# Optimization experiments

Measured on AMD Instinct MI355X. Metric: run time of the kernel, lower is better.

## Reference

```python
import jax, jax.numpy as jnp
import numpy as np

# Production-scale graph dims (see shape_source)
N = 50000      # nodes
E = 800000     # edges (avg degree 16)
C_IN = 128     # input feature dim
H = 96         # hidden (per species: prey X and predator Y)
C_OUT = 40     # num_classes
L = 5          # LVConv layers
DT = 0.05      # integration step


def setup_inputs() -> dict:
    key = jax.random.key(0)
    ks = jax.random.split(key, 14)
    x = jax.random.normal(ks[0], (N, C_IN), jnp.float32)
    edge_index = jax.random.randint(ks[1], (2, E), 0, N, dtype=jnp.int32)
    # lift linears
    Wx = jax.random.normal(ks[2], (C_IN, H), jnp.float32) / np.sqrt(C_IN)
    bx = jnp.zeros((H,), jnp.float32)
    Wy = jax.random.normal(ks[3], (C_IN, H), jnp.float32) / np.sqrt(C_IN)
    by = jnp.zeros((H,), jnp.float32)
    # per-layer Lotka-Volterra coefficients (per-channel), small positive scale
    alpha = 0.1 * jax.random.uniform(ks[4], (L, H), jnp.float32)
    beta  = 0.1 * jax.random.uniform(ks[5], (L, H), jnp.float32)
    gamma = 0.1 * jax.random.uniform(ks[6], (L, H), jnp.float32)
    delta = 0.1 * jax.random.uniform(ks[7], (L, H), jnp.float32)
    # readout on concat([X, Y])
    Wr = jax.random.normal(ks[8], (2 * H, C_OUT), jnp.float32) / np.sqrt(2 * H)
    br = jnp.zeros((C_OUT,), jnp.float32)
    return {"x": x, "edge_index": edge_index, "Wx": Wx, "bx": bx,
            "Wy": Wy, "by": by, "alpha": alpha, "beta": beta,
            "gamma": gamma, "delta": delta, "Wr": Wr, "br": br}


def reference(x, edge_index, Wx, bx, Wy, by, alpha, beta, gamma, delta, Wr, br):
    src, dst = edge_index[0], edge_index[1]
    # in-degree for mean aggregation over incoming edges
    deg = jax.ops.segment_sum(jnp.ones((E,), x.dtype), dst, num_segments=N)
    deg_inv = (1.0 / jnp.maximum(deg, 1.0))[:, None]  # [N,1]

    def mean_agg(v):  # [N,H] -> [N,H] neighbor mean (src -> dst)
        return jax.ops.segment_sum(v[src], dst, num_segments=N) * deg_inv

    # lift to prey (X) and predator (Y) populations
    X = jnp.tanh(x @ Wx + bx)
    Y = jnp.tanh(x @ Wy + by)
    # dropout is identity in eval mode (training=False)
    for l in range(L):
        aggX = mean_agg(X)
        aggY = mean_agg(Y)
        # explicit-Euler Lotka-Volterra dynamics on the graph
        Xn = X + DT * X * (alpha[l] - beta[l] * aggY)
        Yn = Y + DT * Y * (-gamma[l] + delta[l] * aggX)
        X, Y = Xn, Yn
    h = jnp.concatenate([X, Y], axis=-1)  # [N, 2H]
    return h @ Wr + br
```

## Files before the change

### kernel.cpp

```cpp
#include <hip/hip_runtime.h>
#include <hip/hip_bf16.h>
#include <hip/hip_fp16.h>


#define HDIM 96
#define CIN 128
#define COUT 40
#define NLAYER 5
#define DTC 0.05f

#define BK_SHIFT 7
#define BK_SIZE 128
#define EPB 2048
#define BCAP 3072
#define BSTRIDE 3584

typedef float  vfloat2 __attribute__((ext_vector_type(2)));
typedef float  vfloat4 __attribute__((ext_vector_type(4)));
typedef short  vshort8 __attribute__((ext_vector_type(8)));

__device__ __forceinline__ unsigned bf16_rne(float f) {
    unsigned u = __float_as_uint(f);
    return (u + 0x7fffu + ((u >> 16) & 1u)) >> 16;
}

__device__ __forceinline__ unsigned pack_bf16_pair(float xf, float yf) {
    return bf16_rne(xf) | (bf16_rne(yf) << 16);
}

__device__ __forceinline__ unsigned pack_f16_pair(float a, float b) {
    unsigned ha = (unsigned)__half_as_ushort(__float2half_rn(a));
    unsigned hb = (unsigned)__half_as_ushort(__float2half_rn(b));
    return ha | (hb << 16);
}

__device__ __forceinline__ float f16_lo(unsigned u) {
    return __half2float(__ushort_as_half((unsigned short)(u & 0xffffu)));
}
__device__ __forceinline__ float f16_hi(unsigned u) {
    return __half2float(__ushort_as_half((unsigned short)(u >> 16)));
}

__device__ __forceinline__ unsigned pack_fp8_quad(float x0, float y0, float x1, float y1) {
    int lo = __builtin_amdgcn_cvt_pk_fp8_f32(x0, y0, 0, false);
    int full = __builtin_amdgcn_cvt_pk_fp8_f32(x1, y1, lo, true);
    return (unsigned)full;
}

__device__ __forceinline__ float fast_tanh(float x) {
    float e = __expf(2.0f * x);
    return 1.0f - 2.0f * __builtin_amdgcn_rcpf(e + 1.0f);
}


__global__ __launch_bounds__(256) void wprep_kernel(
    const float* __restrict__ Wx, const float* __restrict__ bx,
    const float* __restrict__ Wy, const float* __restrict__ by,
    unsigned short* __restrict__ WcT, float* __restrict__ bc,
    int* __restrict__ gcur, int NB,
    unsigned* __restrict__ Fz0, unsigned* __restrict__ Fz1) {
    int t = blockIdx.x * blockDim.x + threadIdx.x;
    if (t < NB) gcur[t] = 0;
    if (t < 192 * 128) {
        int cc = t >> 7;
        int k = t & 127;
        int h = cc >> 1;
        float w = (cc & 1) ? Wy[k * HDIM + h] : Wx[k * HDIM + h];
        WcT[cc * 128 + k] = (unsigned short)bf16_rne(w);
    }
    if (t < 192) {
        int h = t >> 1;
        bc[t] = (t & 1) ? by[h] : bx[h];
    }
    if (blockIdx.x == 0 && threadIdx.x < 48) {
        Fz0[threadIdx.x] = 0u;
        Fz1[threadIdx.x] = 0u;
    }
}


__global__ __launch_bounds__(256) void bscatter_kernel(
    const int* __restrict__ src, const int* __restrict__ dst,
    int* __restrict__ gcur, unsigned* __restrict__ packed, int E, int NB) {
    __shared__ int h[512];
    __shared__ int cur[512];
    for (int i = threadIdx.x; i < NB; i += 256) h[i] = 0;
    __syncthreads();
    int base = blockIdx.x * EPB;
    int end = min(E, base + EPB);
    for (int e = base + threadIdx.x; e < end; e += 256)
        atomicAdd(&h[dst[e] >> BK_SHIFT], 1);
    __syncthreads();
    for (int i = threadIdx.x; i < NB; i += 256)
        cur[i] = h[i] ? atomicAdd(&gcur[i], h[i]) : 0;
    __syncthreads();
    for (int e = base + threadIdx.x; e < end; e += 256) {
        int d = dst[e];
        int b = d >> BK_SHIFT;
        int pos = atomicAdd(&cur[b], 1);
        if (pos < BCAP)
            packed[(size_t)b * BCAP + pos] =
                (unsigned)src[e] | ((unsigned)(d & (BK_SIZE - 1)) << 17);
    }
}


__global__ __launch_bounds__(256) void bcsr_kernel(
    const unsigned* __restrict__ packed, const int* __restrict__ gcur,
    uint2* __restrict__ rowinfo, int* __restrict__ csr, int N, int NB) {
    __shared__ int ldeg[BK_SIZE];
    __shared__ int sscan[BK_SIZE];
    __shared__ int lcur[BK_SIZE];
    int b = blockIdx.x;
    int t = threadIdx.x;
    int cnt = min(gcur[b], BCAP);
    const unsigned* pk = packed + (size_t)b * BCAP;
    int wbase = b * BSTRIDE;
    if (t < BK_SIZE) ldeg[t] = 0;
    __syncthreads();
    for (int e = t; e < cnt; e += 256)
        atomicAdd(&ldeg[(pk[e] >> 17) & (BK_SIZE - 1)], 1);
    __syncthreads();
    int deg = 0, pad = 0;
    if (t < BK_SIZE) {
        deg = ldeg[t];
        pad = (deg + 3) & ~3;
        sscan[t] = pad;
    }
    __syncthreads();
    for (int off = 1; off < BK_SIZE; off <<= 1) {
        int tv = (t < BK_SIZE && t >= off) ? sscan[t - off] : 0;
        __syncthreads();
        if (t < BK_SIZE) sscan[t] += tv;
        __syncthreads();
    }
    int gpos = 0;
    if (t < BK_SIZE) {
        gpos = wbase + sscan[t] - pad;
        lcur[t] = gpos;
        int node = b * BK_SIZE + t;
        if (node < N) {
            rowinfo[node] = make_uint2(
                (unsigned)gpos | ((unsigned)(pad >> 2) << 21),
                __float_as_uint(1.0f / fmaxf((float)deg, 1.0f)));
        }
    }
    __syncthreads();
    for (int e = t; e < cnt; e += 256) {
        unsigned p = pk[e];
        int l = (p >> 17) & (BK_SIZE - 1);
        int pos = atomicAdd(&lcur[l], 1);
        csr[pos] = (int)(p & 0x1FFFFu);
    }
    __syncthreads();
    if (t < BK_SIZE) {
        for (int p = lcur[t]; p < gpos + pad; p++) csr[p] = N;
    }
}


#define LW_STRIDE 136
#define TILE_STRIDE 200

__global__ __launch_bounds__(256) void lift_mfma_kernel(
    const float* __restrict__ x, const unsigned short* __restrict__ WcT,
    const float* __restrict__ bc, unsigned* __restrict__ S,
    unsigned* __restrict__ F, int N) {
    __shared__ __align__(16) char smem[192 * LW_STRIDE * 2];
    __shared__ float sBc[192];
    unsigned short* sW = (unsigned short*)smem;
    unsigned short* tile = (unsigned short*)smem;
    int t = threadIdx.x;

    {
        const unsigned* g = (const unsigned*)WcT;
        unsigned* s = (unsigned*)sW;
        for (int i = t; i < 192 * 64; i += 256) {
            int cc = i >> 6;
            int kp = i & 63;
            s[cc * (LW_STRIDE / 2) + kp] = g[i];
        }
    }
    if (t < 192) sBc[t] = bc[t];
    __syncthreads();

    int wv = t >> 6;
    int lane = t & 63;
    int quad = lane >> 4;
    int m = lane & 15;
    int mbase = blockIdx.x * 64 + wv * 16;

    int anode = mbase + m;
    if (anode >= N) anode = N - 1;
    const float* xrow = x + (size_t)anode * CIN;

    vfloat4 acc[12];
#pragma unroll
    for (int i = 0; i < 12; i++) acc[i] = (vfloat4){0.f, 0.f, 0.f, 0.f};

#pragma unroll
    for (int kt = 0; kt < 4; kt++) {
        int k0 = kt * 32 + quad * 8;
        float4 xa = *(const float4*)(xrow + k0);
        float4 xb = *(const float4*)(xrow + k0 + 4);
        uint4 ua;
        ua.x = pack_bf16_pair(xa.x, xa.y);
        ua.y = pack_bf16_pair(xa.z, xa.w);
        ua.z = pack_bf16_pair(xb.x, xb.y);
        ua.w = pack_bf16_pair(xb.z, xb.w);
        vshort8 a = *(vshort8*)&ua;
#pragma unroll
        for (int nt = 0; nt < 12; nt++) {
            vshort8 b = *(const vshort8*)&sW[(nt * 16 + m) * LW_STRIDE + k0];
            acc[nt] = __builtin_amdgcn_mfma_f32_16x16x32_bf16(a, b, acc[nt], 0, 0, 0);
        }
    }

    __syncthreads();
#pragma unroll
    for (int nt = 0; nt < 12; nt++) {
        int ccb = nt * 16 + m;
        float bco = sBc[ccb];
#pragma unroll
        for (int r = 0; r < 4; r++) {
            int nl = wv * 16 + quad * 4 + r;
            float v = fast_tanh(acc[nt][r] + bco);
            tile[nl * TILE_STRIDE + ccb] = __half_as_ushort(__float2half_rn(v));
        }
    }
    __syncthreads();

    int nbase = blockIdx.x * 64;
#pragma unroll
    for (int i = 0; i < 6; i++) {
        int idx = i * 256 + t;
        int nl = idx / 24;
        int pos = idx - nl * 24;
        int node = nbase + nl;
        uint4 u = *(const uint4*)&tile[nl * TILE_STRIDE + pos * 8];
        if (node < N) {
            *(uint4*)(S + (size_t)node * 96 + pos * 4) = u;
            float f0 = f16_lo(u.x), f1 = f16_hi(u.x);
            float f2 = f16_lo(u.y), f3 = f16_hi(u.y);
            float f4 = f16_lo(u.z), f5 = f16_hi(u.z);
            float f6 = f16_lo(u.w), f7 = f16_hi(u.w);
            uint2 fq = make_uint2(pack_fp8_quad(f0, f1, f2, f3),
                                  pack_fp8_quad(f4, f5, f6, f7));
            *(uint2*)(F + (size_t)node * 48 + pos * 2) = fq;
        }
    }
}


__global__ __launch_bounds__(256) void layer_kernel(
    const unsigned* __restrict__ F, const unsigned* __restrict__ S,
    unsigned* __restrict__ Sn, unsigned* __restrict__ Fn,
    const uint2* __restrict__ rowinfo, const int* __restrict__ csr,
    const float* __restrict__ alpha, const float* __restrict__ beta,
    const float* __restrict__ gamma, const float* __restrict__ delta,
    int N) {
    int wave = threadIdx.x >> 6;
    int lane = threadIdx.x & 63;
    int li = lane & 15;
    int gbase = lane & 48;

    int node = (blockIdx.x * 4 + wave) * 4 + (lane >> 4);
    bool nvalid = node < N;
    int nclamp = nvalid ? node : N - 1;
    uint2 ri = rowinfo[nclamp];
    int beg = (int)(ri.x & 0x1FFFFFu);
    int cnt = nvalid ? (int)((ri.x >> 21) << 2) : 0;
    float dinv = __uint_as_float(ri.y);

    const uint2* srow = (const uint2*)(S + (size_t)nclamp * 96);
    uint2 su0 = srow[3 * li + 0];
    uint2 su1 = srow[3 * li + 1];
    uint2 su2 = srow[3 * li + 2];

    vfloat2 ac2[6];
#pragma unroll
    for (int i = 0; i < 6; i++) ac2[i] = (vfloat2){0.f, 0.f};

#define UNP(u, k)                                                           \
    do {                                                                    \
        vfloat2 p0 = __builtin_amdgcn_cvt_pk_f32_fp8((int)(u), false);      \
        vfloat2 p1 = __builtin_amdgcn_cvt_pk_f32_fp8((int)(u), true);       \
        ac2[2*(k)+0] += p0; ac2[2*(k)+1] += p1;                             \
    } while (0)
#define UNP3(u)  do { UNP((u).x, 0); UNP((u).y, 1); UNP((u).z, 2); } while (0)

    for (int base = 0; base < cnt; base += 64) {
        int rem = min(cnt - base, 64);
        int4 my = {0, 0, 0, 0};
        if (li * 4 < rem) my = *(const int4*)(csr + beg + base + 4 * li);
        int j = 0;
        for (; j + 8 <= rem; j += 8) {
            int l0 = gbase + (j >> 2);
            int s0 = __shfl(my.x, l0);
            int s1 = __shfl(my.y, l0);
            int s2 = __shfl(my.z, l0);
            int s3 = __shfl(my.w, l0);
            int s4 = __shfl(my.x, l0 + 1);
            int s5 = __shfl(my.y, l0 + 1);
            int s6 = __shfl(my.z, l0 + 1);
            int s7 = __shfl(my.w, l0 + 1);
            uint3 u0 = ((const uint3*)(F + (size_t)s0 * 48))[li];
            uint3 u1 = ((const uint3*)(F + (size_t)s1 * 48))[li];
            uint3 u2 = ((const uint3*)(F + (size_t)s2 * 48))[li];
            uint3 u3 = ((const uint3*)(F + (size_t)s3 * 48))[li];
            uint3 u4 = ((const uint3*)(F + (size_t)s4 * 48))[li];
            uint3 u5 = ((const uint3*)(F + (size_t)s5 * 48))[li];
            uint3 u6 = ((const uint3*)(F + (size_t)s6 * 48))[li];
            uint3 u7 = ((const uint3*)(F + (size_t)s7 * 48))[li];
            UNP3(u0); UNP3(u1); UNP3(u2); UNP3(u3);
            UNP3(u4); UNP3(u5); UNP3(u6); UNP3(u7);
        }
        if (j < rem) {
            int l0 = gbase + (j >> 2);
            int s0 = __shfl(my.x, l0);
            int s1 = __shfl(my.y, l0);
            int s2 = __shfl(my.z, l0);
            int s3 = __shfl(my.w, l0);
            uint3 u0 = ((const uint3*)(F + (size_t)s0 * 48))[li];
            uint3 u1 = ((const uint3*)(F + (size_t)s1 * 48))[li];
            uint3 u2 = ((const uint3*)(F + (size_t)s2 * 48))[li];
            uint3 u3 = ((const uint3*)(F + (size_t)s3 * 48))[li];
            UNP3(u0); UNP3(u1); UNP3(u2); UNP3(u3);
        }
    }
#undef UNP3
#undef UNP

    if (!nvalid) return;

    unsigned so[6];
    unsigned fo[3];
#pragma unroll
    for (int k = 0; k < 3; k++) {
        int p = 3 * li + k;
        float2 a2 = ((const float2*)alpha)[p];
        float2 b2 = ((const float2*)beta)[p];
        float2 g2 = ((const float2*)gamma)[p];
        float2 d2 = ((const float2*)delta)[p];
        uint2 su = (k == 0) ? su0 : (k == 1) ? su1 : su2;
        float vx = f16_lo(su.x), vy = f16_hi(su.x);
        float vz = f16_lo(su.y), vw = f16_hi(su.y);
        float ox = vx + DTC * vx * (a2.x - b2.x * (ac2[2*k].y * dinv));
        float oy = vy + DTC * vy * (-g2.x + d2.x * (ac2[2*k].x * dinv));
        float oz = vz + DTC * vz * (a2.y - b2.y * (ac2[2*k+1].y * dinv));
        float ow = vw + DTC * vw * (-g2.y + d2.y * (ac2[2*k+1].x * dinv));
        so[2*k+0] = pack_f16_pair(ox, oy);
        so[2*k+1] = pack_f16_pair(oz, ow);
        fo[k] = pack_fp8_quad(ox, oy, oz, ow);
    }
    {
        uint3 t0 = {so[0], so[1], so[2]};
        uint3 t1 = {so[3], so[4], so[5]};
        ((uint3*)(Sn + (size_t)node * 96))[2*li+0] = t0;
        ((uint3*)(Sn + (size_t)node * 96))[2*li+1] = t1;
    }
    if (Fn) {
        uint3 tf = {fo[0], fo[1], fo[2]};
        ((uint3*)(Fn + (size_t)node * 48))[li] = tf;
    }
}


#define WG_STRIDE 200

__global__ __launch_bounds__(256) void readout_mfma_kernel(
    const unsigned short* __restrict__ sh, const float* __restrict__ Wr,
    const float* __restrict__ br, float* __restrict__ out, int N) {
    __shared__ unsigned short sW[48 * WG_STRIDE];
    __shared__ float sB[48];
    int t = threadIdx.x;

    for (int i = t; i < 48 * 192; i += 256) {
        int n = i / 192;
        int kk = i - n * 192;
        int h = kk >> 1;
        float w = 0.f;
        if (n < COUT) w = (kk & 1) ? Wr[(HDIM + h) * COUT + n] : Wr[h * COUT + n];
        sW[n * WG_STRIDE + kk] = __half_as_ushort(__float2half_rn(w));
    }
    if (t < 48) sB[t] = (t < COUT) ? br[t] : 0.f;
    __syncthreads();

    int wv = t >> 6;
    int lane = t & 63;
    int quad = lane >> 4;
    int m = lane & 15;
    int mbase = blockIdx.x * 64 + wv * 16;

    int anode = mbase + m;
    if (anode >= N) anode = N - 1;
    const unsigned short* arow = sh + (size_t)anode * 192;

    vfloat4 acc0 = {0.f, 0.f, 0.f, 0.f};
    vfloat4 acc1 = {0.f, 0.f, 0.f, 0.f};
    vfloat4 acc2 = {0.f, 0.f, 0.f, 0.f};

#pragma unroll
    for (int kt = 0; kt < 6; kt++) {
        int k0 = kt * 32 + quad * 8;
        vshort8 a = *(const vshort8*)(arow + k0);
        vshort8 b0 = *(const vshort8*)&sW[(0 * 16 + m) * WG_STRIDE + k0];
        vshort8 b1 = *(const vshort8*)&sW[(1 * 16 + m) * WG_STRIDE + k0];
        vshort8 b2 = *(const vshort8*)&sW[(2 * 16 + m) * WG_STRIDE + k0];
        acc0 = __builtin_amdgcn_mfma_f32_16x16x32_f16(a, b0, acc0, 0, 0, 0);
        acc1 = __builtin_amdgcn_mfma_f32_16x16x32_f16(a, b1, acc1, 0, 0, 0);
        acc2 = __builtin_amdgcn_mfma_f32_16x16x32_f16(a, b2, acc2, 0, 0, 0);
    }

    float bo0 = sB[m];
    float bo1 = sB[16 + m];
    float bo2 = (m < 8) ? sB[32 + m] : 0.f;
#pragma unroll
    for (int r = 0; r < 4; r++) {
        int node = mbase + quad * 4 + r;
        if (node < N) {
            float* orow = out + (size_t)node * COUT;
            orow[m] = acc0[r] + bo0;
            orow[16 + m] = acc1[r] + bo1;
            if (m < 8) orow[32 + m] = acc2[r] + bo2;
        }
    }
}


extern "C" void kernel_launch(void* const* d_in, const int* in_sizes, int n_in,
                              void* d_out, int out_size, void* d_ws, size_t ws_size,
                              hipStream_t stream) {
    const float* x     = (const float*)d_in[0];
    const int*   ei    = (const int*)d_in[1];
    const float* Wx    = (const float*)d_in[2];
    const float* bx    = (const float*)d_in[3];
    const float* Wy    = (const float*)d_in[4];
    const float* by    = (const float*)d_in[5];
    const float* alpha = (const float*)d_in[6];
    const float* beta  = (const float*)d_in[7];
    const float* gamma = (const float*)d_in[8];
    const float* delta = (const float*)d_in[9];
    const float* Wr    = (const float*)d_in[10];
    const float* br    = (const float*)d_in[11];

    const int N = in_sizes[0] / CIN;
    const int E = in_sizes[1] / 2;
    const int NB = (N + BK_SIZE - 1) >> BK_SHIFT;
    const int nchunk = (E + EPB - 1) / EPB;

    char* ws = (char*)d_ws;
    size_t off = 0;
    auto alloc = [&](size_t bytes) -> void* {
        off = (off + 255) & ~(size_t)255;
        void* p = ws + off;
        off += bytes;
        return p;
    };
    int* gcur          = (int*)alloc((size_t)NB * sizeof(int));
    unsigned* pckd     = (unsigned*)alloc((size_t)NB * BCAP * sizeof(unsigned));
    uint2* rowinfo     = (uint2*)alloc((size_t)N * sizeof(uint2));
    int* csr           = (int*)alloc(((size_t)NB * BSTRIDE + 64) * sizeof(int));
    unsigned* Sa   = (unsigned*)alloc((size_t)N * 96 * sizeof(unsigned));
    unsigned* Sb   = (unsigned*)alloc((size_t)N * 96 * sizeof(unsigned));
    unsigned* Fa   = (unsigned*)alloc((size_t)(N + 1) * 48 * sizeof(unsigned));
    unsigned* Fb   = (unsigned*)alloc((size_t)(N + 1) * 48 * sizeof(unsigned));
    unsigned short* WcT = (unsigned short*)alloc((size_t)192 * 128 * sizeof(unsigned short));
    float* bc      = (float*)alloc((size_t)192 * sizeof(float));
    (void)ws_size;

    const int* e_src = ei;
    const int* e_dst = ei + E;

    wprep_kernel<<<(192 * 128 + 255) / 256, 256, 0, stream>>>(
        Wx, bx, Wy, by, WcT, bc, gcur, NB,
        Fa + (size_t)N * 48, Fb + (size_t)N * 48);

    bscatter_kernel<<<nchunk, 256, 0, stream>>>(e_src, e_dst, gcur, pckd, E, NB);
    bcsr_kernel<<<NB, 256, 0, stream>>>(pckd, gcur, rowinfo, csr, N, NB);

    lift_mfma_kernel<<<(N + 63) / 64, 256, 0, stream>>>(x, WcT, bc, Sa, Fa, N);

    const unsigned* Sc = Sa;
    unsigned* Snx = Sb;
    const unsigned* Fc = Fa;
    unsigned* Fnx = Fb;
    for (int l = 0; l < NLAYER; l++) {
        bool last = (l == NLAYER - 1);
        layer_kernel<<<(N + 15) / 16, 256, 0, stream>>>(
            Fc, Sc, Snx, last ? (unsigned*)nullptr : Fnx,
            rowinfo, csr,
            alpha + l * HDIM, beta + l * HDIM, gamma + l * HDIM, delta + l * HDIM, N);
        const unsigned* ts = Sc; Sc = Snx; Snx = (unsigned*)ts;
        const unsigned* tf = Fc; Fc = Fnx; Fnx = (unsigned*)tf;
    }

    readout_mfma_kernel<<<(N + 63) / 64, 256, 0, stream>>>(
        (const unsigned short*)Sc, Wr, br, (float*)d_out, N);
}
```

Baseline: 304.9 us.

## Split fp8 gather features into three channel planes and launch per-plane blocks

Stores the fp8 neighbor feature buffer as three planes of 16 words per node instead of one 48-word row. The layer kernel is launched with three times as many blocks, each gathering a single dword per lane from one plane. This shrinks each plane's working set so it fits better in L2/MALL during the random gather, and gives more parallelism. In exchange, CSR traversal and index shuffles are repeated three times per node, and each gathered load is narrower.

```diff
diff --git a/kernel.cpp b/kernel.cpp
--- a/kernel.cpp
+++ b/kernel.cpp
@@ -58,7 +58,7 @@
     const float* __restrict__ Wy, const float* __restrict__ by,
     unsigned short* __restrict__ WcT, float* __restrict__ bc,
     int* __restrict__ gcur, int NB,
-    unsigned* __restrict__ Fz0, unsigned* __restrict__ Fz1) {
+    unsigned* __restrict__ F0, unsigned* __restrict__ F1, int N) {
     int t = blockIdx.x * blockDim.x + threadIdx.x;
     if (t < NB) gcur[t] = 0;
     if (t < 192 * 128) {
@@ -73,8 +73,10 @@
         bc[t] = (t & 1) ? by[h] : bx[h];
     }
     if (blockIdx.x == 0 && threadIdx.x < 48) {
-        Fz0[threadIdx.x] = 0u;
-        Fz1[threadIdx.x] = 0u;
+        int plane = threadIdx.x >> 4, d = threadIdx.x & 15;
+        size_t o = ((size_t)plane * (N + 1) + N) * 16 + d;
+        F0[o] = 0u;
+        F1[o] = 0u;
     }
 }
 
@@ -246,7 +248,9 @@
             float f6 = f16_lo(u.w), f7 = f16_hi(u.w);
             uint2 fq = make_uint2(pack_fp8_quad(f0, f1, f2, f3),
                                   pack_fp8_quad(f4, f5, f6, f7));
-            *(uint2*)(F + (size_t)node * 48 + pos * 2) = fq;
+            int plane = pos >> 3;
+            int slot = (2 * pos) & 15;
+            *(uint2*)(F + ((size_t)plane * (N + 1) + node) * 16 + slot) = fq;
         }
     }
 }
@@ -258,13 +262,19 @@
     const uint2* __restrict__ rowinfo, const int* __restrict__ csr,
     const float* __restrict__ alpha, const float* __restrict__ beta,
     const float* __restrict__ gamma, const float* __restrict__ delta,
-    int N) {
+    int N, int nblk) {
+    int bid = blockIdx.x;
+    int plane = bid / nblk;
+    int tile = bid - plane * nblk;
+    size_t pstride = (size_t)(N + 1) * 16;
+    const unsigned* Fp = F + (size_t)plane * pstride;
+
     int wave = threadIdx.x >> 6;
     int lane = threadIdx.x & 63;
     int li = lane & 15;
     int gbase = lane & 48;
 
-    int node = (blockIdx.x * 4 + wave) * 4 + (lane >> 4);
+    int node = (tile * 4 + wave) * 4 + (lane >> 4);
     bool nvalid = node < N;
     int nclamp = nvalid ? node : N - 1;
     uint2 ri = rowinfo[nclamp];
@@ -272,22 +282,14 @@
     int cnt = nvalid ? (int)((ri.x >> 21) << 2) : 0;
     float dinv = __uint_as_float(ri.y);
 
-    const uint2* srow = (const uint2*)(S + (size_t)nclamp * 96);
-    uint2 su0 = srow[3 * li + 0];
-    uint2 su1 = srow[3 * li + 1];
-    uint2 su2 = srow[3 * li + 2];
-
-    vfloat2 ac2[6];
-#pragma unroll
-    for (int i = 0; i < 6; i++) ac2[i] = (vfloat2){0.f, 0.f};
-
-#define UNP(u, k)                                                           \
+    vfloat2 a0 = (vfloat2){0.f, 0.f};
+    vfloat2 a1 = (vfloat2){0.f, 0.f};
+
+#define UNP(u)                                                              \
     do {                                                                    \
-        vfloat2 p0 = __builtin_amdgcn_cvt_pk_f32_fp8((int)(u), false);      \
-        vfloat2 p1 = __builtin_amdgcn_cvt_pk_f32_fp8((int)(u), true);       \
-        ac2[2*(k)+0] += p0; ac2[2*(k)+1] += p1;                             \
+        a0 += __builtin_amdgcn_cvt_pk_f32_fp8((int)(u), false);             \
+        a1 += __builtin_amdgcn_cvt_pk_f32_fp8((int)(u), true);              \
     } while (0)
-#define UNP3(u)  do { UNP((u).x, 0); UNP((u).y, 1); UNP((u).z, 2); } while (0)
 
     for (int base = 0; base < cnt; base += 64) {
         int rem = min(cnt - base, 64);
@@ -304,16 +306,16 @@
             int s5 = __shfl(my.y, l0 + 1);
             int s6 = __shfl(my.z, l0 + 1);
             int s7 = __shfl(my.w, l0 + 1);
-            uint3 u0 = ((const uint3*)(F + (size_t)s0 * 48))[li];
-            uint3 u1 = ((const uint3*)(F + (size_t)s1 * 48))[li];
-            uint3 u2 = ((const uint3*)(F + (size_t)s2 * 48))[li];
-            uint3 u3 = ((const uint3*)(F + (size_t)s3 * 48))[li];
-            uint3 u4 = ((const uint3*)(F + (size_t)s4 * 48))[li];
-            uint3 u5 = ((const uint3*)(F + (size_t)s5 * 48))[li];
-            uint3 u6 = ((const uint3*)(F + (size_t)s6 * 48))[li];
-            uint3 u7 = ((const uint3*)(F + (size_t)s7 * 48))[li];
-            UNP3(u0); UNP3(u1); UNP3(u2); UNP3(u3);
-            UNP3(u4); UNP3(u5); UNP3(u6); UNP3(u7);
+            unsigned u0 = Fp[(size_t)s0 * 16 + li];
+            unsigned u1 = Fp[(size_t)s1 * 16 + li];
+            unsigned u2 = Fp[(size_t)s2 * 16 + li];
+            unsigned u3 = Fp[(size_t)s3 * 16 + li];
+            unsigned u4 = Fp[(size_t)s4 * 16 + li];
+            unsigned u5 = Fp[(size_t)s5 * 16 + li];
+            unsigned u6 = Fp[(size_t)s6 * 16 + li];
+            unsigned u7 = Fp[(size_t)s7 * 16 + li];
+            UNP(u0); UNP(u1); UNP(u2); UNP(u3);
+            UNP(u4); UNP(u5); UNP(u6); UNP(u7);
         }
         if (j < rem) {
             int l0 = gbase + (j >> 2);
@@ -321,48 +323,33 @@
             int s1 = __shfl(my.y, l0);
             int s2 = __shfl(my.z, l0);
             int s3 = __shfl(my.w, l0);
-            uint3 u0 = ((const uint3*)(F + (size_t)s0 * 48))[li];
-            uint3 u1 = ((const uint3*)(F + (size_t)s1 * 48))[li];
-            uint3 u2 = ((const uint3*)(F + (size_t)s2 * 48))[li];
-            uint3 u3 = ((const uint3*)(F + (size_t)s3 * 48))[li];
-            UNP3(u0); UNP3(u1); UNP3(u2); UNP3(u3);
-        }
-    }
-#undef UNP3
+            unsigned u0 = Fp[(size_t)s0 * 16 + li];
+            unsigned u1 = Fp[(size_t)s1 * 16 + li];
+            unsigned u2 = Fp[(size_t)s2 * 16 + li];
+            unsigned u3 = Fp[(size_t)s3 * 16 + li];
+            UNP(u0); UNP(u1); UNP(u2); UNP(u3);
+        }
+    }
 #undef UNP
 
     if (!nvalid) return;
 
-    unsigned so[6];
-    unsigned fo[3];
-#pragma unroll
-    for (int k = 0; k < 3; k++) {
-        int p = 3 * li + k;
-        float2 a2 = ((const float2*)alpha)[p];
-        float2 b2 = ((const float2*)beta)[p];
-        float2 g2 = ((const float2*)gamma)[p];
-        float2 d2 = ((const float2*)delta)[p];
-        uint2 su = (k == 0) ? su0 : (k == 1) ? su1 : su2;
-        float vx = f16_lo(su.x), vy = f16_hi(su.x);
-        float vz = f16_lo(su.y), vw = f16_hi(su.y);
-        float ox = vx + DTC * vx * (a2.x - b2.x * (ac2[2*k].y * dinv));
-        float oy = vy + DTC * vy * (-g2.x + d2.x * (ac2[2*k].x * dinv));
-        float oz = vz + DTC * vz * (a2.y - b2.y * (ac2[2*k+1].y * dinv));
-        float ow = vw + DTC * vw * (-g2.y + d2.y * (ac2[2*k+1].x * dinv));
-        so[2*k+0] = pack_f16_pair(ox, oy);
-        so[2*k+1] = pack_f16_pair(oz, ow);
-        fo[k] = pack_fp8_quad(ox, oy, oz, ow);
-    }
-    {
-        uint3 t0 = {so[0], so[1], so[2]};
-        uint3 t1 = {so[3], so[4], so[5]};
-        ((uint3*)(Sn + (size_t)node * 96))[2*li+0] = t0;
-        ((uint3*)(Sn + (size_t)node * 96))[2*li+1] = t1;
-    }
-    if (Fn) {
-        uint3 tf = {fo[0], fo[1], fo[2]};
-        ((uint3*)(Fn + (size_t)node * 48))[li] = tf;
-    }
+    int h0 = plane * 32 + 2 * li;
+    float2 a2 = *(const float2*)(alpha + h0);
+    float2 b2 = *(const float2*)(beta + h0);
+    float2 g2 = *(const float2*)(gamma + h0);
+    float2 d2 = *(const float2*)(delta + h0);
+    uint2 su = *(const uint2*)(S + (size_t)node * 96 + h0);
+    float vx = f16_lo(su.x), vy = f16_hi(su.x);
+    float vz = f16_lo(su.y), vw = f16_hi(su.y);
+    float ox = vx + DTC * vx * (a2.x - b2.x * (a0.y * dinv));
+    float oy = vy + DTC * vy * (-g2.x + d2.x * (a0.x * dinv));
+    float oz = vz + DTC * vz * (a2.y - b2.y * (a1.y * dinv));
+    float ow = vw + DTC * vw * (-g2.y + d2.y * (a1.x * dinv));
+    uint2 so = make_uint2(pack_f16_pair(ox, oy), pack_f16_pair(oz, ow));
+    *(uint2*)(Sn + (size_t)node * 96 + h0) = so;
+    if (Fn) Fn[(size_t)plane * pstride + (size_t)node * 16 + li] =
+        pack_fp8_quad(ox, oy, oz, ow);
 }
 
 
@@ -448,6 +435,7 @@
     const int E = in_sizes[1] / 2;
     const int NB = (N + BK_SIZE - 1) >> BK_SHIFT;
     const int nchunk = (E + EPB - 1) / EPB;
+    const int nblk = (N + 15) / 16;
 
     char* ws = (char*)d_ws;
     size_t off = 0;
@@ -473,8 +461,7 @@
     const int* e_dst = ei + E;
 
     wprep_kernel<<<(192 * 128 + 255) / 256, 256, 0, stream>>>(
-        Wx, bx, Wy, by, WcT, bc, gcur, NB,
-        Fa + (size_t)N * 48, Fb + (size_t)N * 48);
+        Wx, bx, Wy, by, WcT, bc, gcur, NB, Fa, Fb, N);
 
     bscatter_kernel<<<nchunk, 256, 0, stream>>>(e_src, e_dst, gcur, pckd, E, NB);
     bcsr_kernel<<<NB, 256, 0, stream>>>(pckd, gcur, rowinfo, csr, N, NB);
@@ -487,10 +474,11 @@
     unsigned* Fnx = Fb;
     for (int l = 0; l < NLAYER; l++) {
         bool last = (l == NLAYER - 1);
-        layer_kernel<<<(N + 15) / 16, 256, 0, stream>>>(
+        layer_kernel<<<3 * nblk, 256, 0, stream>>>(
             Fc, Sc, Snx, last ? (unsigned*)nullptr : Fnx,
             rowinfo, csr,
-            alpha + l * HDIM, beta + l * HDIM, gamma + l * HDIM, delta + l * HDIM, N);
+            alpha + l * HDIM, beta + l * HDIM, gamma + l * HDIM, delta + l * HDIM,
+            N, nblk);
         const unsigned* ts = Sc; Sc = Snx; Snx = (unsigned*)ts;
         const unsigned* tf = Fc; Fc = Fnx; Fnx = (unsigned*)tf;
     }
```

After: 285.3 us. 6.4% less time.
